# Kernel optimization log

Measured on AMD Instinct MI355X. Metric: run time of the kernel, lower is better.

## Reference

```python
import jax, jax.numpy as jnp
import numpy as np

N_NODES = 100000
N_EDGES = 1600000
IN_FEATS = 64
H_FEATS = 64
NUM_CLASSES = 32


def _cgnn(h, e, src, dst, W, b, n_nodes):
    # message: m = h[src] * e  (e is [E,1], broadcasts over feature dim)
    m = h[src] * e  # [E, F]
    # segment mean over destination nodes (DGL fn.mean -> 0 for isolated nodes)
    s = jax.ops.segment_sum(m, dst, num_segments=n_nodes)  # [N, F]
    deg = jax.ops.segment_sum(jnp.ones((m.shape[0],), m.dtype), dst,
                              num_segments=n_nodes)  # [N]
    h_N = s / jnp.maximum(deg, 1.0)[:, None]
    h_total = jnp.concatenate([h, h_N], axis=1)  # [N, 2F]
    return h_total @ W + b


def setup_inputs() -> dict:
    key = jax.random.key(0)
    k = jax.random.split(key, 8)
    in_feat = jax.random.normal(k[0], (N_NODES, IN_FEATS), dtype=jnp.float32)
    edge_feat = jax.random.uniform(k[1], (N_EDGES, 1), dtype=jnp.float32)
    src = jax.random.randint(k[2], (N_EDGES,), 0, N_NODES)
    dst = jax.random.randint(k[3], (N_EDGES,), 0, N_NODES)
    # Linear(2*in_feats, h_feats) and Linear(2*h_feats, num_classes)
    s1 = 1.0 / np.sqrt(2 * IN_FEATS)
    s2 = 1.0 / np.sqrt(2 * H_FEATS)
    W1 = jax.random.uniform(k[4], (2 * IN_FEATS, H_FEATS), jnp.float32, -s1, s1)
    b1 = jax.random.uniform(k[5], (H_FEATS,), jnp.float32, -s1, s1)
    W2 = jax.random.uniform(k[6], (2 * H_FEATS, NUM_CLASSES), jnp.float32, -s2, s2)
    b2 = jax.random.uniform(k[7], (NUM_CLASSES,), jnp.float32, -s2, s2)
    return {"in_feat": in_feat, "edge_feat": edge_feat, "src": src,
            "dst": dst, "W1": W1, "b1": b1, "W2": W2, "b2": b2}


def reference(in_feat, edge_feat, src, dst, W1, b1, W2, b2):
    h = _cgnn(in_feat, edge_feat, src, dst, W1, b1, N_NODES)
    h = jax.nn.relu(h)
    h = _cgnn(h, edge_feat, src, dst, W2, b2, N_NODES)
    return h
```

## Files before the change

### kernel.cpp

```cpp
#include <hip/hip_runtime.h>
#include <hip/hip_bf16.h>


#define F 64
#define EPT 8
#define TPB 1024
#define EPB (EPT * TPB)
#define SBSHIFT 8
#define SBSZ 256
#define NSBMAX 512
#define PADSB 4864

__device__ __forceinline__ unsigned bf16_rne(float f)
{
    unsigned u = __float_as_uint(f);
    return (u + 0x7FFFu + ((u >> 16) & 1u)) >> 16;
}

__global__ __launch_bounds__(256) void cvt_init_kernel(
    const float* __restrict__ x, unsigned short* __restrict__ y, int n8,
    int* __restrict__ bcursor, int nsb)
{
    const int i = blockIdx.x * 256 + threadIdx.x;
    if (i < nsb) bcursor[i] = i * PADSB;
    if (i >= n8) return;
    const float4 a = ((const float4*)x)[2 * i];
    const float4 b = ((const float4*)x)[2 * i + 1];
    uint4 o;
    o.x = bf16_rne(a.x) | (bf16_rne(a.y) << 16);
    o.y = bf16_rne(a.z) | (bf16_rne(a.w) << 16);
    o.z = bf16_rne(b.x) | (bf16_rne(b.y) << 16);
    o.w = bf16_rne(b.z) | (bf16_rne(b.w) << 16);
    ((uint4*)y)[i] = o;
}

__global__ __launch_bounds__(TPB) void multisplit_kernel(
    const int* __restrict__ src, const int* __restrict__ dst,
    const float* __restrict__ ef, int* __restrict__ bcursor,
    int2* __restrict__ brec, int n_edges, int nsb)
{
    __shared__ int lcnt[NSBMAX];
    __shared__ int lbase[NSBMAX];
    const int tid = threadIdx.x;
    for (int i = tid; i < nsb; i += TPB) lcnt[i] = 0;
    __syncthreads();

    const int e0 = blockIdx.x * EPB + tid;
    int d[EPT], rk[EPT];
#pragma unroll
    for (int k = 0; k < EPT; ++k) {
        const int e = e0 + k * TPB;
        const int dd = (e < n_edges) ? dst[e] : -1;
        d[k]  = dd;
        rk[k] = (dd >= 0) ? atomicAdd(&lcnt[dd >> SBSHIFT], 1) : 0;
    }
    __syncthreads();
    for (int i = tid; i < nsb; i += TPB) {
        const int c = lcnt[i];
        lbase[i] = c ? atomicAdd(&bcursor[i], c) : 0;
    }
    __syncthreads();
#pragma unroll
    for (int k = 0; k < EPT; ++k) {
        const int e = e0 + k * TPB;
        if (e < n_edges) {
            const int dd  = d[k];
            const int bkt = dd >> SBSHIFT;
            const int pos = lbase[bkt] + rk[k];
            if (pos < (bkt + 1) * PADSB)
                brec[pos] = make_int2(((dd & (SBSZ - 1)) << 17) | src[e],
                                      __float_as_int(ef[e]));
        }
    }
}

__global__ __launch_bounds__(512) void bucket_sort_kernel(
    int2* __restrict__ brec, const int* __restrict__ bcursor,
    int* __restrict__ off2, int* __restrict__ end2,
    float* __restrict__ invdeg, int n_nodes)
{
    __shared__ int2 stage[PADSB];
    __shared__ int  lcnt[SBSZ];
    __shared__ int  lcur[SBSZ];
    __shared__ int  wsum[4];

    const int b   = blockIdx.x;
    const int tid = threadIdx.x;
    const int w0  = b * PADSB;
    int cnt = bcursor[b] - w0;
    if (cnt > PADSB) cnt = PADSB;

    if (tid < SBSZ) lcnt[tid] = 0;
    __syncthreads();

    for (int i = tid; i < cnt; i += 512) {
        const int2 r = brec[w0 + i];
        stage[i] = r;
        atomicAdd(&lcnt[r.x >> 17], 1);
    }
    __syncthreads();

    int v = 0, c = 0;
    if (tid < SBSZ) {
        c = lcnt[tid];
        v = c;
        for (int d = 1; d < 64; d <<= 1) {
            int t = __shfl_up(v, d, 64);
            if ((tid & 63) >= d) v += t;
        }
        if ((tid & 63) == 63) wsum[tid >> 6] = v;
    }
    __syncthreads();
    if (tid == 0) {
        int a = 0;
#pragma unroll
        for (int i = 0; i < 4; ++i) { int t = wsum[i]; wsum[i] = a; a += t; }
    }
    __syncthreads();
    if (tid < SBSZ) {
        const int excl = wsum[tid >> 6] + (v - c);
        lcur[tid] = excl;
        const int node = (b << SBSHIFT) + tid;
        if (node < n_nodes) {
            off2[node]   = w0 + excl;
            end2[node]   = w0 + excl + c;
            invdeg[node] = 1.0f / fmaxf((float)c, 1.0f);
        }
    }
    __syncthreads();

    for (int i = tid; i < cnt; i += 512) {
        const int2 r   = stage[i];
        const int  pos = atomicAdd(&lcur[r.x >> 17], 1);
        brec[w0 + pos] = make_int2((r.x & 0x1FFFF) << 7, r.y);
    }
}

__global__ __launch_bounds__(256) void agg_kernel(
    const unsigned short* __restrict__ hb, const int2* __restrict__ rec,
    const int* __restrict__ off, const int* __restrict__ end,
    const float* __restrict__ invdeg, unsigned short* __restrict__ sb,
    int n_nodes)
{
    const int wid  = (blockIdx.x * 256 + threadIdx.x) >> 6;
    const int lane = threadIdx.x & 63;
    const int n    = lane >> 5;
    const int r    = lane & 31;
    const int g    = r >> 3;
    const int q    = r & 7;

    const int  node   = wid * 2 + n;
    const bool active = node < n_nodes;
    const int  e0 = active ? off[node] : 0;
    const int  e1 = active ? end[node] : 0;

    const char* __restrict__ hq = (const char*)hb + q * 16;

    float4 aA0 = make_float4(0.f, 0.f, 0.f, 0.f);
    float4 aA1 = make_float4(0.f, 0.f, 0.f, 0.f);
    float4 aB0 = make_float4(0.f, 0.f, 0.f, 0.f);
    float4 aB1 = make_float4(0.f, 0.f, 0.f, 0.f);
    float4 aC0 = make_float4(0.f, 0.f, 0.f, 0.f);
    float4 aC1 = make_float4(0.f, 0.f, 0.f, 0.f);
    float4 aD0 = make_float4(0.f, 0.f, 0.f, 0.f);
    float4 aD1 = make_float4(0.f, 0.f, 0.f, 0.f);

    for (int base = e0; base < e1; base += 16) {
        const int  eA = base + g;
        const int  eB = base + 4 + g;
        const int  eC = base + 8 + g;
        const int  eD = base + 12 + g;
        const bool vA = eA < e1, vB = eB < e1, vC = eC < e1, vD = eD < e1;
        const int2 rA = rec[vA ? eA : e0];
        const int2 rB = rec[vB ? eB : e0];
        const int2 rC = rec[vC ? eC : e0];
        const int2 rD = rec[vD ? eD : e0];
        const float evA = vA ? __int_as_float(rA.y) : 0.f;
        const float evB = vB ? __int_as_float(rB.y) : 0.f;
        const float evC = vC ? __int_as_float(rC.y) : 0.f;
        const float evD = vD ? __int_as_float(rD.y) : 0.f;
        const uint4 xA = *(const uint4*)(hq + rA.x);
        const uint4 xB = *(const uint4*)(hq + rB.x);
        const uint4 xC = *(const uint4*)(hq + rC.x);
        const uint4 xD = *(const uint4*)(hq + rD.x);

#define ACC8(xa, ev, lo, hi)                                         \
        lo.x = fmaf(__uint_as_float(xa.x << 16),         ev, lo.x);  \
        lo.y = fmaf(__uint_as_float(xa.x & 0xFFFF0000u), ev, lo.y);  \
        lo.z = fmaf(__uint_as_float(xa.y << 16),         ev, lo.z);  \
        lo.w = fmaf(__uint_as_float(xa.y & 0xFFFF0000u), ev, lo.w);  \
        hi.x = fmaf(__uint_as_float(xa.z << 16),         ev, hi.x);  \
        hi.y = fmaf(__uint_as_float(xa.z & 0xFFFF0000u), ev, hi.y);  \
        hi.z = fmaf(__uint_as_float(xa.w << 16),         ev, hi.z);  \
        hi.w = fmaf(__uint_as_float(xa.w & 0xFFFF0000u), ev, hi.w);

        ACC8(xA, evA, aA0, aA1)
        ACC8(xB, evB, aB0, aB1)
        ACC8(xC, evC, aC0, aC1)
        ACC8(xD, evD, aD0, aD1)
#undef ACC8
    }

    float4 a0 = make_float4((aA0.x + aB0.x) + (aC0.x + aD0.x),
                            (aA0.y + aB0.y) + (aC0.y + aD0.y),
                            (aA0.z + aB0.z) + (aC0.z + aD0.z),
                            (aA0.w + aB0.w) + (aC0.w + aD0.w));
    float4 a1 = make_float4((aA1.x + aB1.x) + (aC1.x + aD1.x),
                            (aA1.y + aB1.y) + (aC1.y + aD1.y),
                            (aA1.z + aB1.z) + (aC1.z + aD1.z),
                            (aA1.w + aB1.w) + (aC1.w + aD1.w));

#pragma unroll
    for (int m = 8; m <= 16; m <<= 1) {
        a0.x += __shfl_xor(a0.x, m); a0.y += __shfl_xor(a0.y, m);
        a0.z += __shfl_xor(a0.z, m); a0.w += __shfl_xor(a0.w, m);
        a1.x += __shfl_xor(a1.x, m); a1.y += __shfl_xor(a1.y, m);
        a1.z += __shfl_xor(a1.z, m); a1.w += __shfl_xor(a1.w, m);
    }

    if (g == 0 && active) {
        const float id = invdeg[node];
        uint4 o;
        o.x = bf16_rne(a0.x * id) | (bf16_rne(a0.y * id) << 16);
        o.y = bf16_rne(a0.z * id) | (bf16_rne(a0.w * id) << 16);
        o.z = bf16_rne(a1.x * id) | (bf16_rne(a1.y * id) << 16);
        o.w = bf16_rne(a1.z * id) | (bf16_rne(a1.w * id) << 16);
        *(uint4*)(sb + (size_t)node * F + q * 8) = o;
    }
}

template <int OUT, bool RELU, bool OUT_BF16>
__global__ __launch_bounds__(256) void linear_lds_kernel(
    const unsigned short* __restrict__ hin_b,
    const unsigned short* __restrict__ sb,
    const float* __restrict__ W, const float* __restrict__ b,
    float* __restrict__ out, unsigned short* __restrict__ hb_out, int n_nodes)
{
    constexpr int JT  = OUT / 4;
    constexpr int STR = 132;
    __shared__ float xin[64 * STR];

    const int tid   = threadIdx.x;
    const int node0 = blockIdx.x * 64;

#define STAGE_BF16(srcp, base_off)                                        \
    for (int i = tid; i < 512; i += 256) {                                \
        const int ln = i >> 3, c8 = i & 7;                                \
        const int node = node0 + ln;                                     \
        uint4 v = make_uint4(0u, 0u, 0u, 0u);                             \
        if (node < n_nodes)                                               \
            v = *(const uint4*)&srcp[(size_t)node * F + c8 * 8];          \
        float4 lo = make_float4(__uint_as_float(v.x << 16),               \
                                __uint_as_float(v.x & 0xFFFF0000u),       \
                                __uint_as_float(v.y << 16),               \
                                __uint_as_float(v.y & 0xFFFF0000u));      \
        float4 hi = make_float4(__uint_as_float(v.z << 16),               \
                                __uint_as_float(v.z & 0xFFFF0000u),       \
                                __uint_as_float(v.w << 16),               \
                                __uint_as_float(v.w & 0xFFFF0000u));      \
        *(float4*)&xin[ln * STR + (base_off) + c8 * 8]     = lo;          \
        *(float4*)&xin[ln * STR + (base_off) + c8 * 8 + 4] = hi;          \
    }

    STAGE_BF16(hin_b, 0)
    STAGE_BF16(sb,    F)
#undef STAGE_BF16
    __syncthreads();

    const int lane = tid & 63;
    const int j0   = __builtin_amdgcn_readfirstlane((tid >> 6) * JT);

    float acc[JT];
#pragma unroll
    for (int j = 0; j < JT; ++j) acc[j] = b[j0 + j];

    const float* __restrict__ xrow = &xin[lane * STR];
#pragma unroll 2
    for (int k4 = 0; k4 < 32; ++k4) {
        const float4 xv = *(const float4*)&xrow[k4 * 4];
#pragma unroll
        for (int kk = 0; kk < 4; ++kk) {
            const int   k  = k4 * 4 + kk;
            const float xk = ((const float*)&xv)[kk];
#pragma unroll
            for (int j = 0; j < JT; ++j)
                acc[j] = fmaf(xk, W[k * OUT + j0 + j], acc[j]);
        }
    }

    const int node = node0 + lane;
    if (node < n_nodes) {
#pragma unroll
        for (int j = 0; j < JT; ++j) {
            float v = acc[j];
            if (RELU) v = fmaxf(v, 0.f);
            acc[j] = v;
        }
        if constexpr (OUT_BF16) {
            unsigned* __restrict__ hw =
                (unsigned*)(hb_out + (size_t)node * OUT + j0);
#pragma unroll
            for (int j = 0; j < JT; j += 2)
                hw[j >> 1] = bf16_rne(acc[j]) | (bf16_rne(acc[j + 1]) << 16);
        } else {
#pragma unroll
            for (int j = 0; j < JT; ++j)
                out[(size_t)node * OUT + j0 + j] = acc[j];
        }
    }
}

extern "C" void kernel_launch(void* const* d_in, const int* in_sizes, int n_in,
                              void* d_out, int out_size, void* d_ws, size_t ws_size,
                              hipStream_t stream)
{
    const float* in_feat   = (const float*)d_in[0];
    const float* edge_feat = (const float*)d_in[1];
    const int*   src       = (const int*)d_in[2];
    const int*   dst       = (const int*)d_in[3];
    const float* W1        = (const float*)d_in[4];
    const float* b1        = (const float*)d_in[5];
    const float* W2        = (const float*)d_in[6];
    const float* b2        = (const float*)d_in[7];
    float*       out       = (float*)d_out;

    const int n_nodes = in_sizes[0] / F;
    const int n_edges = in_sizes[2];
    const int nsb     = (n_nodes + SBSZ - 1) >> SBSHIFT;

    const int S = 100352;
    int*   wsi     = (int*)d_ws;
    int*   bcursor = wsi;
    int*   off2    = wsi + 1024;
    int*   end2    = wsi + 1024 + S;
    float* invdeg  = (float*)(wsi + 1024 + 2 * S);
    int2*  brec    = (int2*)(wsi + 1024 + 3 * S);
    unsigned short* sb  = (unsigned short*)(brec + (size_t)nsb * PADSB);
    unsigned short* hb0 = sb  + (size_t)n_nodes * F;
    unsigned short* hb1 = hb0 + (size_t)n_nodes * F;

    const int n8    = (n_nodes * F) >> 3;
    const int cgrid = (n8 + 255) / 256;
    const int egrid = (n_edges + EPB - 1) / EPB;
    const int agrid = (n_nodes + 7) / 8;
    const int lgrid = (n_nodes + 63) / 64;

    cvt_init_kernel<<<cgrid, 256, 0, stream>>>(in_feat, hb0, n8, bcursor, nsb);
    multisplit_kernel<<<egrid, TPB, 0, stream>>>(src, dst, edge_feat,
                                                 bcursor, brec, n_edges, nsb);
    bucket_sort_kernel<<<nsb, 512, 0, stream>>>(brec, bcursor, off2, end2,
                                                invdeg, n_nodes);

    agg_kernel<<<agrid, 256, 0, stream>>>(hb0, brec, off2, end2, invdeg, sb, n_nodes);
    linear_lds_kernel<64, true, true><<<lgrid, 256, 0, stream>>>(
        hb0, sb, W1, b1, nullptr, hb1, n_nodes);

    agg_kernel<<<agrid, 256, 0, stream>>>(hb1, brec, off2, end2, invdeg, sb, n_nodes);
    linear_lds_kernel<32, false, false><<<lgrid, 256, 0, stream>>>(
        hb1, sb, W2, b2, out, nullptr, n_nodes);
}
```

Measured before the change: 163.2 us.

## Project layer-2 features before aggregation to halve gathered width

Because mean aggregation is linear, layer 2 now multiplies h by the lower half of W2 first (64->32 features) and then aggregates the 32-wide bf16 projection instead of the 64-wide hidden features. This halves the bytes gathered per edge in the second aggregation, at the cost of an extra small GEMM kernel and one more launch. The edge records now hold node*64 byte offsets, shifted left at use for the 64-wide layer. The first aggregation loop also drops from four to two accumulator sets, and projecting before the mean adds a second bf16 rounding step.

```diff
diff --git a/kernel.cpp b/kernel.cpp
--- a/kernel.cpp
+++ b/kernel.cpp
@@ -132,11 +132,11 @@
     for (int i = tid; i < cnt; i += 512) {
         const int2 r   = stage[i];
         const int  pos = atomicAdd(&lcur[r.x >> 17], 1);
-        brec[w0 + pos] = make_int2((r.x & 0x1FFFF) << 7, r.y);
-    }
-}
-
-__global__ __launch_bounds__(256) void agg_kernel(
+        brec[w0 + pos] = make_int2((r.x & 0x1FFFF) << 6, r.y);
+    }
+}
+
+__global__ __launch_bounds__(256) void agg_h_kernel(
     const unsigned short* __restrict__ hb, const int2* __restrict__ rec,
     const int* __restrict__ off, const int* __restrict__ end,
     const float* __restrict__ invdeg, unsigned short* __restrict__ sb,
@@ -160,29 +160,18 @@
     float4 aA1 = make_float4(0.f, 0.f, 0.f, 0.f);
     float4 aB0 = make_float4(0.f, 0.f, 0.f, 0.f);
     float4 aB1 = make_float4(0.f, 0.f, 0.f, 0.f);
-    float4 aC0 = make_float4(0.f, 0.f, 0.f, 0.f);
-    float4 aC1 = make_float4(0.f, 0.f, 0.f, 0.f);
-    float4 aD0 = make_float4(0.f, 0.f, 0.f, 0.f);
-    float4 aD1 = make_float4(0.f, 0.f, 0.f, 0.f);
-
-    for (int base = e0; base < e1; base += 16) {
+
+    for (int base = e0; base < e1; base += 8) {
         const int  eA = base + g;
         const int  eB = base + 4 + g;
-        const int  eC = base + 8 + g;
-        const int  eD = base + 12 + g;
-        const bool vA = eA < e1, vB = eB < e1, vC = eC < e1, vD = eD < e1;
+        const bool vA = eA < e1;
+        const bool vB = eB < e1;
         const int2 rA = rec[vA ? eA : e0];
         const int2 rB = rec[vB ? eB : e0];
-        const int2 rC = rec[vC ? eC : e0];
-        const int2 rD = rec[vD ? eD : e0];
         const float evA = vA ? __int_as_float(rA.y) : 0.f;
         const float evB = vB ? __int_as_float(rB.y) : 0.f;
-        const float evC = vC ? __int_as_float(rC.y) : 0.f;
-        const float evD = vD ? __int_as_float(rD.y) : 0.f;
-        const uint4 xA = *(const uint4*)(hq + rA.x);
-        const uint4 xB = *(const uint4*)(hq + rB.x);
-        const uint4 xC = *(const uint4*)(hq + rC.x);
-        const uint4 xD = *(const uint4*)(hq + rD.x);
+        const uint4 xA = *(const uint4*)(hq + ((size_t)(unsigned)rA.x << 1));
+        const uint4 xB = *(const uint4*)(hq + ((size_t)(unsigned)rB.x << 1));
 
 #define ACC8(xa, ev, lo, hi)                                         \
         lo.x = fmaf(__uint_as_float(xa.x << 16),         ev, lo.x);  \
@@ -196,19 +185,12 @@
 
         ACC8(xA, evA, aA0, aA1)
         ACC8(xB, evB, aB0, aB1)
-        ACC8(xC, evC, aC0, aC1)
-        ACC8(xD, evD, aD0, aD1)
-#undef ACC8
-    }
-
-    float4 a0 = make_float4((aA0.x + aB0.x) + (aC0.x + aD0.x),
-                            (aA0.y + aB0.y) + (aC0.y + aD0.y),
-                            (aA0.z + aB0.z) + (aC0.z + aD0.z),
-                            (aA0.w + aB0.w) + (aC0.w + aD0.w));
-    float4 a1 = make_float4((aA1.x + aB1.x) + (aC1.x + aD1.x),
-                            (aA1.y + aB1.y) + (aC1.y + aD1.y),
-                            (aA1.z + aB1.z) + (aC1.z + aD1.z),
-                            (aA1.w + aB1.w) + (aC1.w + aD1.w));
+    }
+
+    float4 a0 = make_float4(aA0.x + aB0.x, aA0.y + aB0.y,
+                            aA0.z + aB0.z, aA0.w + aB0.w);
+    float4 a1 = make_float4(aA1.x + aB1.x, aA1.y + aB1.y,
+                            aA1.z + aB1.z, aA1.w + aB1.w);
 
 #pragma unroll
     for (int m = 8; m <= 16; m <<= 1) {
@@ -229,6 +211,72 @@
     }
 }
 
+__global__ __launch_bounds__(256) void agg_y_kernel(
+    const unsigned short* __restrict__ yb, const int2* __restrict__ rec,
+    const int* __restrict__ off, const int* __restrict__ end,
+    const float* __restrict__ invdeg, unsigned short* __restrict__ s2b,
+    int n_nodes)
+{
+    const int wid  = (blockIdx.x * 256 + threadIdx.x) >> 6;
+    const int lane = threadIdx.x & 63;
+    const int n    = lane >> 4;
+    const int r    = lane & 15;
+    const int g    = r >> 2;
+    const int q    = r & 3;
+
+    const int  node   = wid * 4 + n;
+    const bool active = node < n_nodes;
+    const int  e0 = active ? off[node] : 0;
+    const int  e1 = active ? end[node] : 0;
+
+    const char* __restrict__ hq = (const char*)yb + q * 16;
+
+    float4 aA0 = make_float4(0.f, 0.f, 0.f, 0.f);
+    float4 aA1 = make_float4(0.f, 0.f, 0.f, 0.f);
+    float4 aB0 = make_float4(0.f, 0.f, 0.f, 0.f);
+    float4 aB1 = make_float4(0.f, 0.f, 0.f, 0.f);
+
+    for (int base = e0; base < e1; base += 8) {
+        const int  eA = base + g;
+        const int  eB = base + 4 + g;
+        const bool vA = eA < e1;
+        const bool vB = eB < e1;
+        const int2 rA = rec[vA ? eA : e0];
+        const int2 rB = rec[vB ? eB : e0];
+        const float evA = vA ? __int_as_float(rA.y) : 0.f;
+        const float evB = vB ? __int_as_float(rB.y) : 0.f;
+        const uint4 xA = *(const uint4*)(hq + (size_t)(unsigned)rA.x);
+        const uint4 xB = *(const uint4*)(hq + (size_t)(unsigned)rB.x);
+
+        ACC8(xA, evA, aA0, aA1)
+        ACC8(xB, evB, aB0, aB1)
+    }
+
+    float4 a0 = make_float4(aA0.x + aB0.x, aA0.y + aB0.y,
+                            aA0.z + aB0.z, aA0.w + aB0.w);
+    float4 a1 = make_float4(aA1.x + aB1.x, aA1.y + aB1.y,
+                            aA1.z + aB1.z, aA1.w + aB1.w);
+
+#pragma unroll
+    for (int m = 4; m <= 8; m <<= 1) {
+        a0.x += __shfl_xor(a0.x, m); a0.y += __shfl_xor(a0.y, m);
+        a0.z += __shfl_xor(a0.z, m); a0.w += __shfl_xor(a0.w, m);
+        a1.x += __shfl_xor(a1.x, m); a1.y += __shfl_xor(a1.y, m);
+        a1.z += __shfl_xor(a1.z, m); a1.w += __shfl_xor(a1.w, m);
+    }
+#undef ACC8
+
+    if (g == 0 && active) {
+        const float id = invdeg[node];
+        uint4 o;
+        o.x = bf16_rne(a0.x * id) | (bf16_rne(a0.y * id) << 16);
+        o.y = bf16_rne(a0.z * id) | (bf16_rne(a0.w * id) << 16);
+        o.z = bf16_rne(a1.x * id) | (bf16_rne(a1.y * id) << 16);
+        o.w = bf16_rne(a1.z * id) | (bf16_rne(a1.w * id) << 16);
+        *(uint4*)(s2b + (size_t)node * 32 + q * 8) = o;
+    }
+}
+
 template <int OUT, bool RELU, bool OUT_BF16>
 __global__ __launch_bounds__(256) void linear_lds_kernel(
     const unsigned short* __restrict__ hin_b,
@@ -243,13 +291,13 @@
     const int tid   = threadIdx.x;
     const int node0 = blockIdx.x * 64;
 
-#define STAGE_BF16(srcp, base_off)                                        \
-    for (int i = tid; i < 512; i += 256) {                                \
-        const int ln = i >> 3, c8 = i & 7;                                \
-        const int node = node0 + ln;                                     \
+#define STAGE_BF16(srcp, base_off, width)                                 \
+    for (int i = tid; i < 64 * ((width) / 8); i += 256) {                 \
+        const int ln = i / ((width) / 8), c8 = i % ((width) / 8);         \
+        const int node = node0 + ln;                                      \
         uint4 v = make_uint4(0u, 0u, 0u, 0u);                             \
         if (node < n_nodes)                                               \
-            v = *(const uint4*)&srcp[(size_t)node * F + c8 * 8];          \
+            v = *(const uint4*)&srcp[(size_t)node * (width) + c8 * 8];    \
         float4 lo = make_float4(__uint_as_float(v.x << 16),               \
                                 __uint_as_float(v.x & 0xFFFF0000u),       \
                                 __uint_as_float(v.y << 16),               \
@@ -262,9 +310,8 @@
         *(float4*)&xin[ln * STR + (base_off) + c8 * 8 + 4] = hi;          \
     }
 
-    STAGE_BF16(hin_b, 0)
-    STAGE_BF16(sb,    F)
-#undef STAGE_BF16
+    STAGE_BF16(hin_b, 0, 64)
+    STAGE_BF16(sb,    F, 64)
     __syncthreads();
 
     const int lane = tid & 63;
@@ -307,6 +354,93 @@
             for (int j = 0; j < JT; ++j)
                 out[(size_t)node * OUT + j0 + j] = acc[j];
         }
+    }
+}
+
+__global__ __launch_bounds__(256) void y2gemm_kernel(
+    const unsigned short* __restrict__ hin_b, const float* __restrict__ Wb,
+    unsigned short* __restrict__ yb2, int n_nodes)
+{
+    constexpr int STR = 68;
+    __shared__ float xin[64 * STR];
+    const int tid   = threadIdx.x;
+    const int node0 = blockIdx.x * 64;
+
+    STAGE_BF16(hin_b, 0, 64)
+    __syncthreads();
+
+    const int lane = tid & 63;
+    const int j0   = __builtin_amdgcn_readfirstlane((tid >> 6) * 8);
+
+    float acc[8];
+#pragma unroll
+    for (int j = 0; j < 8; ++j) acc[j] = 0.f;
+
+    const float* __restrict__ xrow = &xin[lane * STR];
+#pragma unroll 2
+    for (int k4 = 0; k4 < 16; ++k4) {
+        const float4 xv = *(const float4*)&xrow[k4 * 4];
+#pragma unroll
+        for (int kk = 0; kk < 4; ++kk) {
+            const int   k  = k4 * 4 + kk;
+            const float xk = ((const float*)&xv)[kk];
+#pragma unroll
+            for (int j = 0; j < 8; ++j)
+                acc[j] = fmaf(xk, Wb[k * 32 + j0 + j], acc[j]);
+        }
+    }
+
+    const int node = node0 + lane;
+    if (node < n_nodes) {
+        unsigned* __restrict__ hw = (unsigned*)(yb2 + (size_t)node * 32 + j0);
+#pragma unroll
+        for (int j = 0; j < 8; j += 2)
+            hw[j >> 1] = bf16_rne(acc[j]) | (bf16_rne(acc[j + 1]) << 16);
+    }
+}
+
+__global__ __launch_bounds__(256) void lin2h_kernel(
+    const unsigned short* __restrict__ hin_b,
+    const unsigned short* __restrict__ s2b,
+    const float* __restrict__ Wt, const float* __restrict__ b,
+    float* __restrict__ out, int n_nodes)
+{
+    constexpr int STR = 100;
+    __shared__ float xin[64 * STR];
+    const int tid   = threadIdx.x;
+    const int node0 = blockIdx.x * 64;
+
+    STAGE_BF16(hin_b, 0,  64)
+    STAGE_BF16(s2b,   64, 32)
+#undef STAGE_BF16
+    __syncthreads();
+
+    const int lane = tid & 63;
+    const int j0   = __builtin_amdgcn_readfirstlane((tid >> 6) * 8);
+
+    float acc[8];
+#pragma unroll
+    for (int j = 0; j < 8; ++j) acc[j] = b[j0 + j];
+
+    const float* __restrict__ xrow = &xin[lane * STR];
+#pragma unroll 2
+    for (int k4 = 0; k4 < 16; ++k4) {
+        const float4 xv = *(const float4*)&xrow[k4 * 4];
+#pragma unroll
+        for (int kk = 0; kk < 4; ++kk) {
+            const int   k  = k4 * 4 + kk;
+            const float xk = ((const float*)&xv)[kk];
+#pragma unroll
+            for (int j = 0; j < 8; ++j)
+                acc[j] = fmaf(xk, Wt[k * 32 + j0 + j], acc[j]);
+        }
+    }
+
+    const int node = node0 + lane;
+    if (node < n_nodes) {
+#pragma unroll
+        for (int j = 0; j < 8; ++j)
+            out[(size_t)node * 32 + j0 + j] = acc[j] + xrow[64 + j0 + j];
     }
 }
 
@@ -338,12 +472,15 @@
     unsigned short* sb  = (unsigned short*)(brec + (size_t)nsb * PADSB);
     unsigned short* hb0 = sb  + (size_t)n_nodes * F;
     unsigned short* hb1 = hb0 + (size_t)n_nodes * F;
-
-    const int n8    = (n_nodes * F) >> 3;
-    const int cgrid = (n8 + 255) / 256;
-    const int egrid = (n_edges + EPB - 1) / EPB;
-    const int agrid = (n_nodes + 7) / 8;
-    const int lgrid = (n_nodes + 63) / 64;
+    unsigned short* yb2 = hb1 + (size_t)n_nodes * F;
+    unsigned short* s2b = yb2 + (size_t)n_nodes * 32;
+
+    const int n8     = (n_nodes * F) >> 3;
+    const int cgrid  = (n8 + 255) / 256;
+    const int egrid  = (n_edges + EPB - 1) / EPB;
+    const int agrid1 = (n_nodes + 7) / 8;
+    const int agrid2 = (n_nodes + 15) / 16;
+    const int lgrid  = (n_nodes + 63) / 64;
 
     cvt_init_kernel<<<cgrid, 256, 0, stream>>>(in_feat, hb0, n8, bcursor, nsb);
     multisplit_kernel<<<egrid, TPB, 0, stream>>>(src, dst, edge_feat,
@@ -351,11 +488,13 @@
     bucket_sort_kernel<<<nsb, 512, 0, stream>>>(brec, bcursor, off2, end2,
                                                 invdeg, n_nodes);
 
-    agg_kernel<<<agrid, 256, 0, stream>>>(hb0, brec, off2, end2, invdeg, sb, n_nodes);
+    agg_h_kernel<<<agrid1, 256, 0, stream>>>(hb0, brec, off2, end2, invdeg,
+                                             sb, n_nodes);
     linear_lds_kernel<64, true, true><<<lgrid, 256, 0, stream>>>(
         hb0, sb, W1, b1, nullptr, hb1, n_nodes);
 
-    agg_kernel<<<agrid, 256, 0, stream>>>(hb1, brec, off2, end2, invdeg, sb, n_nodes);
-    linear_lds_kernel<32, false, false><<<lgrid, 256, 0, stream>>>(
-        hb1, sb, W2, b2, out, nullptr, n_nodes);
-}
+    y2gemm_kernel<<<lgrid, 256, 0, stream>>>(hb1, W2 + 64 * 32, yb2, n_nodes);
+    agg_y_kernel<<<agrid2, 256, 0, stream>>>(yb2, brec, off2, end2, invdeg,
+                                             s2b, n_nodes);
+    lin2h_kernel<<<lgrid, 256, 0, stream>>>(hb1, s2b, W2, b2, out, n_nodes);
+}
```

Measured after the change: 153.1 us (median of 5 runs). 6.2% less time.
